# Kernel optimization log

Hardware: AMD Instinct MI355X
Metric: run time of the kernel (lower is better)

The kernel has to match this reference:

```python
import jax, jax.numpy as jnp
import numpy as np

M, D, G, E = 100000, 64, 1024, 1600000  # nodes, hidden, graphs, edges


def setup_inputs() -> dict:
    key = jax.random.key(0)
    k1, k2, k3, k4 = jax.random.split(key, 4)
    x = jax.random.normal(k1, (M, D), dtype=jnp.float32)
    batch = jnp.sort(jax.random.randint(k2, (M,), 0, G)).astype(jnp.int64)
    edge = jax.random.randint(k3, (2, E), 0, M).astype(jnp.int64)
    # nn.Linear(D, 1) parameters
    att_w = jax.random.normal(k4, (1, D), dtype=jnp.float32) * (1.0 / np.sqrt(D))
    att_b = jnp.zeros((1,), dtype=jnp.float32)
    return {"x": x, "att_w": att_w, "att_b": att_b, "batch": batch, "edge": edge}


def reference(x, att_w, att_b, batch, edge):
    # imp = attention(x): [M, 1] -> [M]
    imp = (x @ att_w.T + att_b)[:, 0]
    # scatter_softmax of imp over graph segments (batch)
    seg_max = jax.ops.segment_max(imp, batch, num_segments=G)
    e = jnp.exp(imp - seg_max[batch])
    denom = jax.ops.segment_sum(e, batch, num_segments=G)
    a = e / denom[batch]  # [M]
    # (degree branch is dead code when degree=False; degree softmax unused)
    # per-node weighted outer product imp_k * x_k x_k^T, scatter-summed per graph
    wj = (a[:, None] * x)[:, :, None] * x[:, None, :]  # [M, D, D]
    out = jax.ops.segment_sum(wj, batch, num_segments=G)  # [G, D, D]
    # Triuvec: upper-triangular (incl. diagonal) vectorization, row-major
    iu = jnp.triu_indices(D)
    return out[:, iu[0], iu[1]]  # [G, D*(D+1)/2]
```

## Files before the change

kernel.cpp:

```cpp
#include <hip/hip_runtime.h>
#include <hip/hip_bf16.h>
#include <math.h>


#define DDIM 64
#define NTRI 2080
#define TK   32

typedef __bf16 bf16x8 __attribute__((ext_vector_type(8)));
typedef float  f32x4  __attribute__((ext_vector_type(4)));

__device__ __forceinline__ unsigned pack_bf16(float a, float b) {
    __hip_bfloat162 h2 = __float22bfloat162_rn(make_float2(a, b));
    return *reinterpret_cast<unsigned*>(&h2);
}

__global__ void __launch_bounds__(256)
bounds_kernel(const int* __restrict__ batch, int* __restrict__ seg_start, int M, int G)
{
    const int m = blockIdx.x * 256 + threadIdx.x;
    if (m >= M) return;
    const int b0 = batch[m];
    if (m == 0) {
        for (int g = 0; g <= b0; ++g) seg_start[g] = 0;
    } else {
        const int bp = batch[m - 1];
        for (int g = bp + 1; g <= b0; ++g) seg_start[g] = m;
    }
    if (m == M - 1) {
        for (int g = b0 + 1; g <= G; ++g) seg_start[g] = M;
    }
}

__global__ void __launch_bounds__(256)
sop_kernel(const float* __restrict__ x,
           const float* __restrict__ att_w,
           const float* __restrict__ att_b,
           const int*   __restrict__ seg_start,
           float*       __restrict__ out)
{
    __shared__ unsigned short sT[2][2][DDIM * TK];
    __shared__ float sRed[8];

    const int g   = blockIdx.x;
    const int tid = threadIdx.x;
    const int s   = seg_start[g];
    const int n   = seg_start[g + 1] - s;
    float* og = out + (size_t)g * NTRI;

    if (n == 0) {
        for (int i = tid; i < NTRI; i += 256) og[i] = 0.f;
        return;
    }

    const float4* x4 = (const float4*)x;
    const int wid  = tid >> 6;
    const int lane = tid & 63;
    const int c    = lane & 15;
    const int q    = lane >> 4;
    const int p    = 4 * wid + q;

    const float4 wv = ((const float4*)att_w)[c];
    const float  bb = att_b[0];

    const int sw   = q ^ ((c >> 2) & 3);
    const int offA = (16 * wid + c) * TK + (sw << 3);
    const int offB = c * TK + (sw << 3);

    f32x4 acc[4];
#pragma unroll
    for (int jt = 0; jt < 4; ++jt) acc[jt] = (f32x4){0.f, 0.f, 0.f, 0.f};

    const int T = (n + TK - 1) / TK;
    float lsum = 0.f;

    float4 p0, p1;
    {
        const int m0 = 2 * p;
        const float4 z = {0.f, 0.f, 0.f, 0.f};
        p0 = (m0     < n) ? x4[(size_t)(s + m0) * 16 + c]     : z;
        p1 = (m0 + 1 < n) ? x4[(size_t)(s + m0 + 1) * 16 + c] : z;
    }

    for (int t = 0; t < T; ++t) {
        const int m0  = t * TK + 2 * p;
        const int cur = t & 1;

        float d0 = fmaf(p0.x, wv.x, fmaf(p0.y, wv.y, fmaf(p0.z, wv.z, p0.w * wv.w)));
        float d1 = fmaf(p1.x, wv.x, fmaf(p1.y, wv.y, fmaf(p1.z, wv.z, p1.w * wv.w)));
#pragma unroll
        for (int mk = 1; mk < 16; mk <<= 1) {
            d0 += __shfl_xor(d0, mk, 16);
            d1 += __shfl_xor(d1, mk, 16);
        }
        float e0 = 0.f, e1 = 0.f;
        if (m0     < n) e0 = __expf(d0 + bb);
        if (m0 + 1 < n) e1 = __expf(d1 + bb);
        lsum += e0 + e1;

        unsigned* A32 = (unsigned*)sT[cur][0];
        unsigned* B32 = (unsigned*)sT[cur][1];
        const float* f0 = (const float*)&p0;
        const float* f1 = (const float*)&p1;
#pragma unroll
        for (int jf = 0; jf < 4; ++jf) {
            const int ui = (4 * c + jf) * 16 + ((wid ^ (c & 3)) << 2) + q;
            A32[ui] = pack_bf16(e0 * f0[jf], e1 * f1[jf]);
            B32[ui] = pack_bf16(f0[jf], f1[jf]);
        }

        if (t + 1 < T) {
            const int m0n = (t + 1) * TK + 2 * p;
            const float4 z = {0.f, 0.f, 0.f, 0.f};
            p0 = (m0n     < n) ? x4[(size_t)(s + m0n) * 16 + c]     : z;
            p1 = (m0n + 1 < n) ? x4[(size_t)(s + m0n + 1) * 16 + c] : z;
        }
        __syncthreads();

        const unsigned short* As = sT[cur][0];
        const unsigned short* Bs = sT[cur][1];
        const bf16x8 av = *(const bf16x8*)(As + offA);
#pragma unroll
        for (int jt = 0; jt < 4; ++jt) {
            const bf16x8 bv = *(const bf16x8*)(Bs + offB + jt * 16 * TK);
            acc[jt] = __builtin_amdgcn_mfma_f32_16x16x32_bf16(av, bv, acc[jt], 0, 0, 0);
        }
    }

#pragma unroll
    for (int off = 32; off > 0; off >>= 1) lsum += __shfl_down(lsum, off, 64);
    if (lane == 0) sRed[wid] = lsum;
    __syncthreads();
    if (tid == 0) sRed[4] = 16.0f / (sRed[0] + sRed[1] + sRed[2] + sRed[3]);
    __syncthreads();
    const float invd = sRed[4];

    const int rbase = 16 * wid + q * 4;
#pragma unroll
    for (int jt = 0; jt < 4; ++jt) {
        const int j = 16 * jt + c;
#pragma unroll
        for (int r = 0; r < 4; ++r) {
            const int i = rbase + r;
            if (j >= i) og[i * DDIM - (i * (i - 1)) / 2 + (j - i)] = acc[jt][r] * invd;
        }
    }
}

extern "C" void kernel_launch(void* const* d_in, const int* in_sizes, int n_in,
                              void* d_out, int out_size, void* d_ws, size_t ws_size,
                              hipStream_t stream) {
    const float* x     = (const float*)d_in[0];
    const float* att_w = (const float*)d_in[1];
    const float* att_b = (const float*)d_in[2];
    const int*   batch = (const int*)d_in[3];
    float* out = (float*)d_out;

    const int M = in_sizes[0] / DDIM;
    const int G = out_size / NTRI;

    int* seg_start = (int*)d_ws;

    bounds_kernel<<<(M + 255) / 256, 256, 0, stream>>>(batch, seg_start, M, G);
    sop_kernel<<<G, 256, 0, stream>>>(x, att_w, att_b, seg_start, out);
}
```

Measured before the change: 90.55 us.

## Fuse segment bounds search into main kernel and widen K tile

Removes the separate bounds kernel launch; each block now finds its segment start and end with a wave-parallel ballot-based search over the sorted batch array. The K tile grows from 32 to 128 nodes per iteration. Each thread issues four independent load pairs up front, and the LDS uses a new XOR swizzle so more MFMAs run per barrier. The double-buffered prefetch is replaced by single buffering with more loads in flight, which trades cross-iteration overlap for more memory-level parallelism and fewer syncs.

```diff
diff --git a/kernel.cpp b/kernel.cpp
--- a/kernel.cpp
+++ b/kernel.cpp
@@ -5,7 +5,7 @@
 
 #define DDIM 64
 #define NTRI 2080
-#define TK   32
+#define TKB  128
 
 typedef __bf16 bf16x8 __attribute__((ext_vector_type(8)));
 typedef float  f32x4  __attribute__((ext_vector_type(4)));
@@ -16,114 +16,130 @@
 }
 
 __global__ void __launch_bounds__(256)
-bounds_kernel(const int* __restrict__ batch, int* __restrict__ seg_start, int M, int G)
-{
-    const int m = blockIdx.x * 256 + threadIdx.x;
-    if (m >= M) return;
-    const int b0 = batch[m];
-    if (m == 0) {
-        for (int g = 0; g <= b0; ++g) seg_start[g] = 0;
-    } else {
-        const int bp = batch[m - 1];
-        for (int g = bp + 1; g <= b0; ++g) seg_start[g] = m;
-    }
-    if (m == M - 1) {
-        for (int g = b0 + 1; g <= G; ++g) seg_start[g] = M;
-    }
-}
-
-__global__ void __launch_bounds__(256)
 sop_kernel(const float* __restrict__ x,
            const float* __restrict__ att_w,
            const float* __restrict__ att_b,
-           const int*   __restrict__ seg_start,
-           float*       __restrict__ out)
+           const int*   __restrict__ batch,
+           float*       __restrict__ out,
+           int M)
 {
-    __shared__ unsigned short sT[2][2][DDIM * TK];
+    __shared__ unsigned short sA[DDIM * TKB];
+    __shared__ unsigned short sB[DDIM * TKB];
     __shared__ float sRed[8];
+    __shared__ int   sBnd[2];
 
-    const int g   = blockIdx.x;
-    const int tid = threadIdx.x;
-    const int s   = seg_start[g];
-    const int n   = seg_start[g + 1] - s;
+    const int g    = blockIdx.x;
+    const int tid  = threadIdx.x;
+    const int wid  = tid >> 6;
+    const int lane = tid & 63;
+    const int c    = lane & 15;
+    const int q    = lane >> 4;
+
+    if (wid < 2) {
+        const int v = g + wid;
+        int lo = 0, hi = M;
+        while (hi - lo > 64) {
+            const int step = (hi - lo + 63) >> 6;
+            const int idx  = lo + lane * step;
+            const int bv   = (idx < hi) ? batch[idx] : 0x7fffffff;
+            const unsigned long long lt = __ballot(bv < v);
+            const int cnt = __popcll(lt);
+            if (cnt == 0) {
+                hi = lo;
+            } else {
+                const int nhi = (cnt < 64) ? (lo + cnt * step) : hi;
+                lo = lo + (cnt - 1) * step + 1;
+                hi = (nhi < hi) ? nhi : hi;
+            }
+        }
+        const int idx = lo + lane;
+        const int bv  = (idx < hi) ? batch[idx] : 0x7fffffff;
+        const int cnt = __popcll(__ballot(bv < v));
+        if (lane == 0) sBnd[wid] = lo + cnt;
+    }
+    __syncthreads();
+
+    const int s = sBnd[0];
+    const int n = sBnd[1] - s;
     float* og = out + (size_t)g * NTRI;
 
     if (n == 0) {
-        for (int i = tid; i < NTRI; i += 256) og[i] = 0.f;
+        const f32x4 z4 = {0.f, 0.f, 0.f, 0.f};
+        for (int i = tid; i < NTRI / 4; i += 256) ((f32x4*)og)[i] = z4;
         return;
     }
 
     const float4* x4 = (const float4*)x;
-    const int wid  = tid >> 6;
-    const int lane = tid & 63;
-    const int c    = lane & 15;
-    const int q    = lane >> 4;
-    const int p    = 4 * wid + q;
-
-    const float4 wv = ((const float4*)att_w)[c];
-    const float  bb = att_b[0];
-
-    const int sw   = q ^ ((c >> 2) & 3);
-    const int offA = (16 * wid + c) * TK + (sw << 3);
-    const int offB = c * TK + (sw << 3);
+    const float4  wv = ((const float4*)att_w)[c];
+    const float   bb = att_b[0];
 
     f32x4 acc[4];
 #pragma unroll
     for (int jt = 0; jt < 4; ++jt) acc[jt] = (f32x4){0.f, 0.f, 0.f, 0.f};
 
-    const int T = (n + TK - 1) / TK;
+    unsigned* A32 = (unsigned*)sA;
+    unsigned* B32 = (unsigned*)sB;
+
+    const int T = (n + TKB - 1) / TKB;
     float lsum = 0.f;
 
-    float4 p0, p1;
-    {
-        const int m0 = 2 * p;
+    for (int t = 0; t < T; ++t) {
+        if (t) __syncthreads();
+
+        const int mbase = t * TKB + 8 * wid + 2 * q;
+        float4 p0[4], p1[4];
+        float  d0[4], d1[4];
         const float4 z = {0.f, 0.f, 0.f, 0.f};
-        p0 = (m0     < n) ? x4[(size_t)(s + m0) * 16 + c]     : z;
-        p1 = (m0 + 1 < n) ? x4[(size_t)(s + m0 + 1) * 16 + c] : z;
-    }
-
-    for (int t = 0; t < T; ++t) {
-        const int m0  = t * TK + 2 * p;
-        const int cur = t & 1;
-
-        float d0 = fmaf(p0.x, wv.x, fmaf(p0.y, wv.y, fmaf(p0.z, wv.z, p0.w * wv.w)));
-        float d1 = fmaf(p1.x, wv.x, fmaf(p1.y, wv.y, fmaf(p1.z, wv.z, p1.w * wv.w)));
+#pragma unroll
+        for (int jj = 0; jj < 4; ++jj) {
+            const int m0 = mbase + 32 * jj;
+            p0[jj] = (m0     < n) ? x4[(size_t)(s + m0) * 16 + c]     : z;
+            p1[jj] = (m0 + 1 < n) ? x4[(size_t)(s + m0 + 1) * 16 + c] : z;
+        }
+#pragma unroll
+        for (int jj = 0; jj < 4; ++jj) {
+            d0[jj] = fmaf(p0[jj].x, wv.x, fmaf(p0[jj].y, wv.y, fmaf(p0[jj].z, wv.z, p0[jj].w * wv.w)));
+            d1[jj] = fmaf(p1[jj].x, wv.x, fmaf(p1[jj].y, wv.y, fmaf(p1[jj].z, wv.z, p1[jj].w * wv.w)));
+        }
 #pragma unroll
         for (int mk = 1; mk < 16; mk <<= 1) {
-            d0 += __shfl_xor(d0, mk, 16);
-            d1 += __shfl_xor(d1, mk, 16);
+#pragma unroll
+            for (int jj = 0; jj < 4; ++jj) {
+                d0[jj] += __shfl_xor(d0[jj], mk, 16);
+                d1[jj] += __shfl_xor(d1[jj], mk, 16);
+            }
         }
-        float e0 = 0.f, e1 = 0.f;
-        if (m0     < n) e0 = __expf(d0 + bb);
-        if (m0 + 1 < n) e1 = __expf(d1 + bb);
-        lsum += e0 + e1;
-
-        unsigned* A32 = (unsigned*)sT[cur][0];
-        unsigned* B32 = (unsigned*)sT[cur][1];
-        const float* f0 = (const float*)&p0;
-        const float* f1 = (const float*)&p1;
 #pragma unroll
-        for (int jf = 0; jf < 4; ++jf) {
-            const int ui = (4 * c + jf) * 16 + ((wid ^ (c & 3)) << 2) + q;
-            A32[ui] = pack_bf16(e0 * f0[jf], e1 * f1[jf]);
-            B32[ui] = pack_bf16(f0[jf], f1[jf]);
-        }
-
-        if (t + 1 < T) {
-            const int m0n = (t + 1) * TK + 2 * p;
-            const float4 z = {0.f, 0.f, 0.f, 0.f};
-            p0 = (m0n     < n) ? x4[(size_t)(s + m0n) * 16 + c]     : z;
-            p1 = (m0n + 1 < n) ? x4[(size_t)(s + m0n + 1) * 16 + c] : z;
+        for (int jj = 0; jj < 4; ++jj) {
+            const int m0 = mbase + 32 * jj;
+            float e0 = 0.f, e1 = 0.f;
+            if (m0     < n) e0 = __expf(d0[jj] + bb);
+            if (m0 + 1 < n) e1 = __expf(d1[jj] + bb);
+            lsum += e0 + e1;
+            const int gg = 4 * jj + wid;
+            const float* f0 = (const float*)&p0[jj];
+            const float* f1 = (const float*)&p1[jj];
+#pragma unroll
+            for (int jf = 0; jf < 4; ++jf) {
+                const int ui = (4 * c + jf) * 64 + (((gg ^ c) & 15) << 2) + q;
+                A32[ui] = pack_bf16(e0 * f0[jf], e1 * f1[jf]);
+                B32[ui] = pack_bf16(f0[jf], f1[jf]);
+            }
         }
         __syncthreads();
 
-        const unsigned short* As = sT[cur][0];
-        const unsigned short* Bs = sT[cur][1];
-        const bf16x8 av = *(const bf16x8*)(As + offA);
+        const int sAx = 4 * wid + (c >> 2);
 #pragma unroll
-        for (int jt = 0; jt < 4; ++jt) {
-            const bf16x8 bv = *(const bf16x8*)(Bs + offB + jt * 16 * TK);
-            acc[jt] = __builtin_amdgcn_mfma_f32_16x16x32_bf16(av, bv, acc[jt], 0, 0, 0);
+        for (int kc = 0; kc < 4; ++kc) {
+            const bf16x8 av = *(const bf16x8*)(sA + (16 * wid + c) * TKB
+                                                  + ((((4 * kc + q) ^ sAx) & 15) << 3));
+#pragma unroll
+            for (int jt = 0; jt < 4; ++jt) {
+                const int sBx = 4 * jt + (c >> 2);
+                const bf16x8 bv = *(const bf16x8*)(sB + (16 * jt + c) * TKB
+                                                      + ((((4 * kc + q) ^ sBx) & 15) << 3));
+                acc[jt] = __builtin_amdgcn_mfma_f32_16x16x32_bf16(av, bv, acc[jt], 0, 0, 0);
+            }
         }
     }
 
@@ -159,8 +175,5 @@
     const int M = in_sizes[0] / DDIM;
     const int G = out_size / NTRI;
 
-    int* seg_start = (int*)d_ws;
-
-    bounds_kernel<<<(M + 255) / 256, 256, 0, stream>>>(batch, seg_start, M, G);
-    sop_kernel<<<G, 256, 0, stream>>>(x, att_w, att_b, seg_start, out);
+    sop_kernel<<<G, 256, 0, stream>>>(x, att_w, att_b, batch, out, M);
 }
```

Result: slower. 93.73 us (+3.5%).
